# Optimization experiments

Measured on AMD Instinct MI355X. Metric: run time of the kernel, lower is better.

The kernel has to match this reference:

```python
import jax, jax.numpy as jnp
import numpy as np

NEG = jnp.float32(-1e30)  # finite stand-in for -inf (grad-safe)
BLANK = 0


def setup_inputs() -> dict:
    key = jax.random.key(0)
    k1, k2, k3, k4 = jax.random.split(key, 4)
    B, T, V, S = 64, 1024, 128, 256
    logits = jax.random.normal(k1, (B, T, V), dtype=jnp.float32)
    log_probs = jax.nn.log_softmax(logits, axis=-1)  # valid log-probs like a model head
    log_probs_length = jax.random.randint(k2, (B,), 768, T + 1)
    text_encoded = jax.random.randint(k3, (B, S), 1, V)  # labels exclude blank=0
    text_encoded_length = jax.random.randint(k4, (B,), 64, S + 1)
    return {
        "log_probs": log_probs,
        "log_probs_length": log_probs_length,
        "text_encoded": text_encoded,
        "text_encoded_length": text_encoded_length,
    }


def _ctc_loss(log_probs, input_lengths, targets, target_lengths):
    """CTC loss, matching torch.nn.CTCLoss(blank=0, reduction='mean', zero_infinity=True)."""
    B, T, V = log_probs.shape
    S = targets.shape[1]
    L2 = 2 * S + 1  # extended label sequence: blank-interleaved

    # extended labels ext[b, s]: blank at even s, target[(s-1)//2] at odd s
    ext = jnp.full((B, L2), BLANK, dtype=targets.dtype)
    ext = ext.at[:, 1::2].set(targets)

    # gather per-step log-prob of each extended label: [B, T, L2]
    lp_ext = jnp.take_along_axis(
        log_probs, jnp.broadcast_to(ext[:, None, :], (B, T, L2)), axis=2
    )

    pos = jnp.arange(L2)
    valid_s = pos[None, :] < (2 * target_lengths[:, None] + 1)  # [B, L2]
    ext_m2 = jnp.pad(ext, ((0, 0), (2, 0)), constant_values=BLANK)[:, :-2]
    # skip transition s-2 -> s allowed only at non-blank (odd) positions with differing labels
    skip_mask = (pos[None, :] >= 2) & (pos[None, :] % 2 == 1) & (ext != ext_m2)

    alpha0 = jnp.full((B, L2), NEG, dtype=log_probs.dtype)
    alpha0 = alpha0.at[:, 0].set(lp_ext[:, 0, 0])
    alpha0 = alpha0.at[:, 1].set(jnp.where(target_lengths > 0, lp_ext[:, 0, 1], NEG))
    alpha0 = jnp.where(valid_s, alpha0, NEG)

    lp_ext_T = jnp.moveaxis(lp_ext, 1, 0)  # [T, B, L2]

    def step(alpha, x):
        lp_t, t = x
        s1 = jnp.pad(alpha, ((0, 0), (1, 0)), constant_values=NEG)[:, :-1]
        s2 = jnp.pad(alpha, ((0, 0), (2, 0)), constant_values=NEG)[:, :-2]
        a = jnp.logaddexp(alpha, s1)
        a = jnp.where(skip_mask, jnp.logaddexp(a, s2), a)
        new = jnp.where(valid_s, a + lp_t, NEG)
        # freeze alpha for samples whose input sequence has ended
        new = jnp.where((t < input_lengths)[:, None], new, alpha)
        return new, None

    alpha, _ = jax.lax.scan(step, alpha0, (lp_ext_T[1:], jnp.arange(1, T)))

    L = target_lengths
    idx1 = (2 * L)[:, None]
    idx0 = jnp.maximum(2 * L - 1, 0)[:, None]
    a_blank = jnp.take_along_axis(alpha, idx1, axis=1)[:, 0]
    a_label = jnp.take_along_axis(alpha, idx0, axis=1)[:, 0]
    ll = jnp.logaddexp(a_blank, jnp.where(L > 0, a_label, NEG))
    loss_b = -ll
    # zero_infinity: zero out infeasible alignments
    loss_b = jnp.where(loss_b > 1e29, jnp.float32(0.0), loss_b)
    # reduction='mean': divide each loss by its target length, then batch-mean
    return jnp.mean(loss_b / jnp.maximum(L, 1).astype(log_probs.dtype))


def reference(log_probs, log_probs_length, text_encoded, text_encoded_length):
    return _ctc_loss(log_probs, log_probs_length, text_encoded, text_encoded_length)
```

## Files before the change

kernel.cpp:

```cpp
#include <hip/hip_runtime.h>

constexpr int B_ = 64;
constexpr int T_ = 1024;
constexpr int V_ = 128;
constexpr int S_ = 256;
constexpr int GRING = 32;
constexpr int ROWF = 384;
constexpr int NGW = 4;
constexpr float INV_LN2 = 1.4426950408889634f;
constexpr float LN2 = 0.6931471805599453f;
constexpr unsigned MAGIC = 0x5AD0F00Du;

#define WG_SCOPE __HIP_MEMORY_SCOPE_WORKGROUP
#define AG_SCOPE __HIP_MEMORY_SCOPE_AGENT

template<int CTRL>
__device__ __forceinline__ float dppf(float x) {
    return __int_as_float(__builtin_amdgcn_update_dpp(
        0, __float_as_int(x), CTRL, 0xF, 0xF, false));
}
constexpr int DPP_WAVE_SHR1 = 0x138;
constexpr int DPP_WAVE_SHL1 = 0x130;
constexpr int DPP_ROW_SHR1  = 0x111;
constexpr int DPP_ROW_SHR2  = 0x112;
constexpr int DPP_ROW_SHR4  = 0x114;
constexpr int DPP_ROW_SHR8  = 0x118;
constexpr int DPP_BCAST15   = 0x142;
constexpr int DPP_BCAST31   = 0x143;

__device__ __forceinline__ void poll_eq(int* p, int want) {
    while (__hip_atomic_load(p, __ATOMIC_RELAXED, WG_SCOPE) != want)
        __builtin_amdgcn_s_sleep(1);
}
__device__ __forceinline__ void poll_ge(int* p, int want) {
    while (__hip_atomic_load(p, __ATOMIC_RELAXED, WG_SCOPE) < want)
        __builtin_amdgcn_s_sleep(1);
}

__device__ __forceinline__ int wave_rescale(float a[10], int& K) {
    float mx = a[0];
    #pragma unroll
    for (int k = 1; k < 10; ++k) mx = fmaxf(mx, a[k]);
    mx = fmaxf(mx, dppf<DPP_ROW_SHR1>(mx));
    mx = fmaxf(mx, dppf<DPP_ROW_SHR2>(mx));
    mx = fmaxf(mx, dppf<DPP_ROW_SHR4>(mx));
    mx = fmaxf(mx, dppf<DPP_ROW_SHR8>(mx));
    mx = fmaxf(mx, dppf<DPP_BCAST15>(mx));
    mx = fmaxf(mx, dppf<DPP_BCAST31>(mx));
    const unsigned mb = (unsigned)__builtin_amdgcn_readlane(__float_as_uint(mx), 63);
    const int ks = (mb != 0u) ? (250 - (int)(mb >> 23)) : 0;
    #pragma unroll
    for (int k = 0; k < 10; ++k) a[k] = ldexpf(a[k], ks);
    K += ks;
    return ks;
}

__global__ __launch_bounds__(1024) void ctc_fused8(
    const float* __restrict__ lp,
    const int* __restrict__ in_len,
    const int* __restrict__ tgt,
    const int* __restrict__ tgt_len,
    float* __restrict__ wloss,
    int* __restrict__ wflag,
    float* __restrict__ out)
{
    const int b    = blockIdx.x;
    const int tid  = threadIdx.x;
    const int wid  = tid >> 6;
    const int lane = tid & 63;

    __shared__ float ringF[GRING * ROWF];
    __shared__ float ringB[GRING * ROWF];
    __shared__ float dumpB[640];
    __shared__ int   tagF[8], tagB[8];
    __shared__ int   consF, consB;
    __shared__ int   KBsh;

    const int L  = tgt_len[b];
    const int Tb = in_len[b];
    const float* lpb = lp + (size_t)b * T_ * V_;
    const int* tg = tgt + b * S_;

    const int tm = (Tb - 2) >> 1;
    const int Uf = tm;
    const int Ub = Tb - 2 - tm;

    if (tid == 0) { consF = 0; consB = 0; }
    if (tid < 8) tagF[tid] = -1;
    else if (tid < 16) tagB[tid - 8] = -1;
    __syncthreads();

    if (wid == 4 || wid == 5 || wid == 8 || wid == 9 || wid == 12 || wid == 13)
        return;

    if (wid >= 2) {
        const int gi  = (wid >> 2) * 2 + (wid & 1);
        const int dir = (gi >= 4) ? 1 : 0;
        const int q   = dir ? (gi - 4) : gi;
        const int U   = dir ? Ub : Uf;
        float* ring   = dir ? ringB : ringF;
        int*   tags   = dir ? tagB  : tagF;
        int*   consp  = dir ? &consB : &consF;

        int   labE[5];
        float vmask[5];
        #pragma unroll
        for (int c = 0; c < 5; ++c) {
            const int j = 5 * lane + c;
            if (j < L) { labE[c] = tg[j]; vmask[c] = 1.0f; }
            else       { labE[c] = 0;     vmask[c] = 0.0f; }
        }

        float vA[4][6], vB[4][6];
        auto issueLoads = [&](float (&v)[4][6], int m) {
            const int n = min(4, U - 4 * m);
            #pragma unroll
            for (int r = 0; r < 4; ++r) {
                if (r < n) {
                    const int u = 4 * m + 1 + r;
                    const int t = dir ? (Tb - 1 - u) : u;
                    const float* row = lpb + (size_t)t * V_;
                    v[r][0] = row[0];
                    #pragma unroll
                    for (int c = 0; c < 5; ++c) v[r][c + 1] = row[labE[c]];
                }
            }
        };
        auto processBlock = [&](float (&v)[4][6], int m) {
            const int n = min(4, U - 4 * m);
            while (__hip_atomic_load(consp, __ATOMIC_RELAXED, WG_SCOPE) < 4 * m - 28)
                __builtin_amdgcn_s_sleep(1);
            #pragma unroll
            for (int r = 0; r < 4; ++r) {
                if (r < n) {
                    const int u = 4 * m + 1 + r;
                    float e[6];
                    e[0] = __builtin_exp2f(v[r][0] * INV_LN2);
                    #pragma unroll
                    for (int c = 0; c < 5; ++c)
                        e[c + 1] = vmask[c] * __builtin_exp2f(v[r][c + 1] * INV_LN2);
                    float* rb = ring + ((u - 1) & (GRING - 1)) * ROWF;
                    ((float2*)rb)[lane]         = make_float2(e[0], e[1]);
                    ((float2*)(rb + 128))[lane] = make_float2(e[2], e[3]);
                    ((float2*)(rb + 256))[lane] = make_float2(e[4], e[5]);
                }
            }
            if (lane == 0)
                __hip_atomic_store(&tags[m & 7], m, __ATOMIC_RELEASE, WG_SCOPE);
        };

        int mA = q;
        bool haveA = (4 * mA + 1 <= U);
        if (haveA) issueLoads(vA, mA);
        while (haveA) {
            const int mB = mA + NGW;
            const bool haveB = (4 * mB + 1 <= U);
            if (haveB) issueLoads(vB, mB);
            processBlock(vA, mA);
            const int mA2 = mB + NGW;
            const bool haveA2 = (4 * mA2 + 1 <= U);
            if (haveA2) issueLoads(vA, mA2);
            if (haveB) processBlock(vB, mB);
            mA = mA2; haveA = haveA2;
        }
        return;
    }

    if (wid == 1) {
        float sB[5];
        #pragma unroll
        for (int c = 0; c < 5; ++c) {
            const int j = 5 * lane + c + 1;
            sB[c] = (j < L && tg[j] != tg[j - 1]) ? 1.0f : 0.0f;
        }
        float g[10];
        #pragma unroll
        for (int k = 0; k < 10; ++k) g[k] = 0.0f;
        {
            const float pb = __builtin_exp2f(lpb[(size_t)(Tb - 1) * V_] * INV_LN2);
            const float pl = __builtin_exp2f(lpb[(size_t)(Tb - 1) * V_ + tg[L - 1]] * INV_LN2);
            #pragma unroll
            for (int k = 0; k < 10; ++k) {
                const int s = 10 * lane + k;
                if (s == 2 * L)     g[k] = pb;
                if (s == 2 * L - 1) g[k] = pl;
            }
        }
        float d0n = dppf<DPP_WAVE_SHL1>(g[0]);
        float d1n = dppf<DPP_WAVE_SHL1>(g[1]);
        int K = 0;

        float2 S0[12], S1[12];
        auto readBlock = [&](float2 (&S)[12], int m) {
            const int base = ((4 * m) & (GRING - 1)) * ROWF + 2 * lane;
            #pragma unroll
            for (int r = 0; r < 4; ++r)
                #pragma unroll
                for (int pl = 0; pl < 3; ++pl)
                    S[r * 3 + pl] = *(const float2*)&ringB[base + r * ROWF + pl * 128];
        };
        auto rowCore = [&](float2 c0, float2 c1, float2 c2) {
            const float d0 = d0n, d1 = d1n;
            const float p0 = c0.x;
            g[0] = (g[0] + g[1]) * p0;
            g[1] = (g[1] + g[2] + sB[0] * g[3]) * c0.y;
            d0n = dppf<DPP_WAVE_SHL1>(g[0]);
            d1n = dppf<DPP_WAVE_SHL1>(g[1]);
            g[2] = (g[2] + g[3]) * p0;
            g[3] = (g[3] + g[4] + sB[1] * g[5]) * c1.x;
            g[4] = (g[4] + g[5]) * p0;
            g[5] = (g[5] + g[6] + sB[2] * g[7]) * c1.y;
            g[6] = (g[6] + g[7]) * p0;
            g[7] = (g[7] + g[8] + sB[3] * g[9]) * c2.x;
            g[8] = (g[8] + g[9]) * p0;
            g[9] = (g[9] + d0 + sB[4] * d1) * c2.y;
        };
        auto row4 = [&](float2 (&S)[12]) {
            #pragma unroll
            for (int r = 0; r < 4; ++r) rowCore(S[r * 3], S[r * 3 + 1], S[r * 3 + 2]);
        };

        const int FB = Ub >> 2;
        poll_eq(&tagB[0], 0); readBlock(S0, 0);
        int mb = 0;
        for (; mb + 2 <= FB; mb += 2) {
            if (mb + 1 < FB) { poll_eq(&tagB[(mb + 1) & 7], mb + 1); readBlock(S1, mb + 1); }
            row4(S0);
            if (lane == 0) __hip_atomic_store(&consB, 4 * mb + 4, __ATOMIC_RELAXED, WG_SCOPE);
            if (mb + 2 < FB) { poll_eq(&tagB[(mb + 2) & 7], mb + 2); readBlock(S0, mb + 2); }
            row4(S1);
            if (lane == 0) __hip_atomic_store(&consB, 4 * mb + 8, __ATOMIC_RELAXED, WG_SCOPE);
            { const int ks = wave_rescale(g, K);
              d0n = ldexpf(d0n, ks); d1n = ldexpf(d1n, ks); }
        }
        if (mb < FB) {
            row4(S0);
            if (lane == 0) __hip_atomic_store(&consB, 4 * mb + 4, __ATOMIC_RELAXED, WG_SCOPE);
            { const int ks = wave_rescale(g, K);
              d0n = ldexpf(d0n, ks); d1n = ldexpf(d1n, ks); }
        }
        for (int u = 4 * FB + 1; u <= Ub; ++u) {
            poll_eq(&tagB[FB & 7], FB);
            const int base = ((u - 1) & (GRING - 1)) * ROWF + 2 * lane;
            rowCore(*(const float2*)&ringB[base],
                    *(const float2*)&ringB[base + 128],
                    *(const float2*)&ringB[base + 256]);
        }

        {
            const float d0 = d0n, d1 = d1n;
            g[0] = g[0] + g[1];
            g[1] = g[1] + g[2] + sB[0] * g[3];
            g[2] = g[2] + g[3];
            g[3] = g[3] + g[4] + sB[1] * g[5];
            g[4] = g[4] + g[5];
            g[5] = g[5] + g[6] + sB[2] * g[7];
            g[6] = g[6] + g[7];
            g[7] = g[7] + g[8] + sB[3] * g[9];
            g[8] = g[8] + g[9];
            g[9] = g[9] + d0 + sB[4] * d1;
        }
        #pragma unroll
        for (int k = 0; k < 10; ++k) dumpB[10 * lane + k] = g[k];
        if (lane == 0) {
            KBsh = K;
            __hip_atomic_store(&consB, Ub + 64, __ATOMIC_RELAXED, WG_SCOPE);
        }
        return;
    }

    float skipf[5];
    #pragma unroll
    for (int c = 0; c < 5; ++c) {
        const int j = 5 * lane + c;
        skipf[c] = (j >= 1 && j < L && tg[j] != tg[j - 1]) ? 1.0f : 0.0f;
    }
    float a[10];
    #pragma unroll
    for (int k = 0; k < 10; ++k) a[k] = 0.0f;
    {
        const float p00 = __builtin_exp2f(lpb[0] * INV_LN2);
        const float p01 = __builtin_exp2f(lpb[tg[0]] * INV_LN2);
        if (lane == 0) { a[0] = p00; a[1] = p01; }
    }
    float u9n = 0.0f;
    int K = 0;

    float2 S0[12], S1[12];
    auto readBlock = [&](float2 (&S)[12], int m) {
        const int base = ((4 * m) & (GRING - 1)) * ROWF + 2 * lane;
        #pragma unroll
        for (int r = 0; r < 4; ++r)
            #pragma unroll
            for (int pl = 0; pl < 3; ++pl)
                S[r * 3 + pl] = *(const float2*)&ringF[base + r * ROWF + pl * 128];
    };
    auto rowCore = [&](float2 c0, float2 c1, float2 c2) {
        const float u9 = u9n;
        const float p0 = c0.x;
        a[9] = (a[9] + a[8] + skipf[4] * a[7]) * c2.y;
        u9n = dppf<DPP_WAVE_SHR1>(a[9]);
        a[8] = (a[8] + a[7]) * p0;
        a[7] = (a[7] + a[6] + skipf[3] * a[5]) * c2.x;
        a[6] = (a[6] + a[5]) * p0;
        a[5] = (a[5] + a[4] + skipf[2] * a[3]) * c1.y;
        a[4] = (a[4] + a[3]) * p0;
        a[3] = (a[3] + a[2] + skipf[1] * a[1]) * c1.x;
        a[2] = (a[2] + a[1]) * p0;
        a[1] = (a[1] + a[0] + skipf[0] * u9) * c0.y;
        a[0] = (a[0] + u9) * p0;
    };
    auto row4 = [&](float2 (&S)[12]) {
        #pragma unroll
        for (int r = 0; r < 4; ++r) rowCore(S[r * 3], S[r * 3 + 1], S[r * 3 + 2]);
    };

    const int FB = Uf >> 2;
    poll_eq(&tagF[0], 0); readBlock(S0, 0);
    int mb = 0;
    for (; mb + 2 <= FB; mb += 2) {
        if (mb + 1 < FB) { poll_eq(&tagF[(mb + 1) & 7], mb + 1); readBlock(S1, mb + 1); }
        row4(S0);
        if (lane == 0) __hip_atomic_store(&consF, 4 * mb + 4, __ATOMIC_RELAXED, WG_SCOPE);
        if (mb + 2 < FB) { poll_eq(&tagF[(mb + 2) & 7], mb + 2); readBlock(S0, mb + 2); }
        row4(S1);
        if (lane == 0) __hip_atomic_store(&consF, 4 * mb + 8, __ATOMIC_RELAXED, WG_SCOPE);
        { const int ks = wave_rescale(a, K); u9n = ldexpf(u9n, ks); }
    }
    if (mb < FB) {
        row4(S0);
        if (lane == 0) __hip_atomic_store(&consF, 4 * mb + 4, __ATOMIC_RELAXED, WG_SCOPE);
        { const int ks = wave_rescale(a, K); u9n = ldexpf(u9n, ks); }
    }
    for (int u = 4 * FB + 1; u <= Uf; ++u) {
        poll_eq(&tagF[FB & 7], FB);
        const int base = ((u - 1) & (GRING - 1)) * ROWF + 2 * lane;
        rowCore(*(const float2*)&ringF[base],
                *(const float2*)&ringF[base + 128],
                *(const float2*)&ringF[base + 256]);
    }
    if (lane == 0) __hip_atomic_store(&consF, Uf + 64, __ATOMIC_RELAXED, WG_SCOPE);

    poll_ge(&consB, Ub + 64);
    double sum = 0.0;
    #pragma unroll
    for (int k = 0; k < 10; ++k)
        sum += (double)a[k] * (double)dumpB[10 * lane + k];
    #pragma unroll
    for (int d = 1; d < 64; d <<= 1) sum += __shfl_xor(sum, d, 64);

    if (lane == 0) {
        float loss = 0.0f;
        if (sum > 0.0) {
            const long long ub2 = __double_as_longlong(sum);
            const int ex = (int)((ub2 >> 52) & 2047) - 1023;
            const double f = __longlong_as_double(
                (ub2 & 0x000FFFFFFFFFFFFFLL) | 0x3FF0000000000000LL);
            const float ll2 = __builtin_log2f((float)f) + (float)(ex - K - KBsh);
            loss = -(ll2 * LN2);
            if (!(loss <= 1e29f)) loss = 0.0f;
        }
        wloss[b] = loss / (float)L;
        __hip_atomic_store(&wflag[b], (int)MAGIC, __ATOMIC_RELEASE, AG_SCOPE);
    }

    if (b == 0) {
        while ((unsigned)__hip_atomic_load(&wflag[lane], __ATOMIC_ACQUIRE, AG_SCOPE) != MAGIC)
            __builtin_amdgcn_s_sleep(1);
        float v = wloss[lane];
        #pragma unroll
        for (int o = 1; o < 64; o <<= 1) v += __shfl_xor(v, o, 64);
        if (lane == 0) out[0] = v / (float)B_;
    }
}

extern "C" void kernel_launch(void* const* d_in, const int* in_sizes, int n_in,
                              void* d_out, int out_size, void* d_ws, size_t ws_size,
                              hipStream_t stream) {
    const float* lp      = (const float*)d_in[0];
    const int*   in_len  = (const int*)d_in[1];
    const int*   tgt     = (const int*)d_in[2];
    const int*   tgt_len = (const int*)d_in[3];
    float* wloss = (float*)d_ws;
    int*   wflag = (int*)((char*)d_ws + 256);
    float* out   = (float*)d_out;

    ctc_fused8<<<B_, 1024, 0, stream>>>(lp, in_len, tgt, tgt_len, wloss, wflag, out);
}
```

Measured before the change: 142.9 us.

## Load full log-prob rows coalesced, gather labels via bpermute, and speculate ring tag polls

Producer waves now load each time step's 128-wide log-prob row as one coalesced float2 per lane. The per-label values are gathered in-register with ds_bpermute instead of six scattered global loads per lane. Consumer waves read the ring tag for the next block before computing the current one and skip the blocking poll when the tag is already set, so the synchronisation latency sits off the critical recurrence. The trade is extra bpermute and select work in the producer in return for fewer uncoalesced loads and less polling stall in the serial alpha and beta loops.

Measured after the change: 142.4 us. About the same (-0.4%).

```diff
diff --git a/kernel.cpp b/kernel.cpp
--- a/kernel.cpp
+++ b/kernel.cpp
@@ -28,6 +28,10 @@
 constexpr int DPP_BCAST15   = 0x142;
 constexpr int DPP_BCAST31   = 0x143;
 
+__device__ __forceinline__ float bperm(int byte_idx, float v) {
+    return __int_as_float(__builtin_amdgcn_ds_bpermute(byte_idx, __float_as_int(v)));
+}
+
 __device__ __forceinline__ void poll_eq(int* p, int want) {
     while (__hip_atomic_load(p, __ATOMIC_RELAXED, WG_SCOPE) != want)
         __builtin_amdgcn_s_sleep(1);
@@ -55,7 +59,7 @@
     return ks;
 }
 
-__global__ __launch_bounds__(1024) void ctc_fused8(
+__global__ __launch_bounds__(1024) void ctc_fused9(
     const float* __restrict__ lp,
     const int* __restrict__ in_len,
     const int* __restrict__ tgt,
@@ -102,31 +106,31 @@
         int*   tags   = dir ? tagB  : tagF;
         int*   consp  = dir ? &consB : &consF;
 
-        int   labE[5];
+        int   bidx[5];
+        float oddc[5];
         float vmask[5];
         #pragma unroll
         for (int c = 0; c < 5; ++c) {
             const int j = 5 * lane + c;
-            if (j < L) { labE[c] = tg[j]; vmask[c] = 1.0f; }
-            else       { labE[c] = 0;     vmask[c] = 0.0f; }
-        }
-
-        float vA[4][6], vB[4][6];
-        auto issueLoads = [&](float (&v)[4][6], int m) {
+            const int lab = (j < L) ? tg[j] : 0;
+            bidx[c]  = (lab >> 1) << 2;
+            oddc[c]  = (lab & 1) ? 1.0f : 0.0f;
+            vmask[c] = (j < L) ? 1.0f : 0.0f;
+        }
+
+        float2 vA[4], vB[4];
+        auto issueLoads = [&](float2 (&v)[4], int m) {
             const int n = min(4, U - 4 * m);
             #pragma unroll
             for (int r = 0; r < 4; ++r) {
                 if (r < n) {
                     const int u = 4 * m + 1 + r;
                     const int t = dir ? (Tb - 1 - u) : u;
-                    const float* row = lpb + (size_t)t * V_;
-                    v[r][0] = row[0];
-                    #pragma unroll
-                    for (int c = 0; c < 5; ++c) v[r][c + 1] = row[labE[c]];
+                    v[r] = ((const float2*)(lpb + (size_t)t * V_))[lane];
                 }
             }
         };
-        auto processBlock = [&](float (&v)[4][6], int m) {
+        auto processBlock = [&](float2 (&v)[4], int m) {
             const int n = min(4, U - 4 * m);
             while (__hip_atomic_load(consp, __ATOMIC_RELAXED, WG_SCOPE) < 4 * m - 28)
                 __builtin_amdgcn_s_sleep(1);
@@ -135,10 +139,14 @@
                 if (r < n) {
                     const int u = 4 * m + 1 + r;
                     float e[6];
-                    e[0] = __builtin_exp2f(v[r][0] * INV_LN2);
+                    e[0] = __builtin_exp2f(bperm(0, v[r].x) * INV_LN2);
                     #pragma unroll
-                    for (int c = 0; c < 5; ++c)
-                        e[c + 1] = vmask[c] * __builtin_exp2f(v[r][c + 1] * INV_LN2);
+                    for (int c = 0; c < 5; ++c) {
+                        const float va = bperm(bidx[c], v[r].x);
+                        const float vb = bperm(bidx[c], v[r].y);
+                        const float val = va + oddc[c] * (vb - va);
+                        e[c + 1] = vmask[c] * __builtin_exp2f(val * INV_LN2);
+                    }
                     float* rb = ring + ((u - 1) & (GRING - 1)) * ROWF;
                     ((float2*)rb)[lane]         = make_float2(e[0], e[1]);
                     ((float2*)(rb + 128))[lane] = make_float2(e[2], e[3]);
@@ -224,14 +232,24 @@
         poll_eq(&tagB[0], 0); readBlock(S0, 0);
         int mb = 0;
         for (; mb + 2 <= FB; mb += 2) {
-            if (mb + 1 < FB) { poll_eq(&tagB[(mb + 1) & 7], mb + 1); readBlock(S1, mb + 1); }
+            if (mb + 1 < FB) readBlock(S1, mb + 1);
+            int spA = (mb + 2 < FB)
+                ? __hip_atomic_load(&tagB[(mb + 2) & 7], __ATOMIC_RELAXED, WG_SCOPE) : 0;
+            __builtin_amdgcn_sched_barrier(0);
             row4(S0);
             if (lane == 0) __hip_atomic_store(&consB, 4 * mb + 4, __ATOMIC_RELAXED, WG_SCOPE);
-            if (mb + 2 < FB) { poll_eq(&tagB[(mb + 2) & 7], mb + 2); readBlock(S0, mb + 2); }
+            if (mb + 2 < FB) {
+                if (spA != mb + 2) poll_eq(&tagB[(mb + 2) & 7], mb + 2);
+                readBlock(S0, mb + 2);
+            }
+            int spB = (mb + 3 < FB)
+                ? __hip_atomic_load(&tagB[(mb + 3) & 7], __ATOMIC_RELAXED, WG_SCOPE) : 0;
+            __builtin_amdgcn_sched_barrier(0);
             row4(S1);
             if (lane == 0) __hip_atomic_store(&consB, 4 * mb + 8, __ATOMIC_RELAXED, WG_SCOPE);
             { const int ks = wave_rescale(g, K);
               d0n = ldexpf(d0n, ks); d1n = ldexpf(d1n, ks); }
+            if (mb + 3 < FB && spB != mb + 3) poll_eq(&tagB[(mb + 3) & 7], mb + 3);
         }
         if (mb < FB) {
             row4(S0);
@@ -319,13 +337,23 @@
     poll_eq(&tagF[0], 0); readBlock(S0, 0);
     int mb = 0;
     for (; mb + 2 <= FB; mb += 2) {
-        if (mb + 1 < FB) { poll_eq(&tagF[(mb + 1) & 7], mb + 1); readBlock(S1, mb + 1); }
+        if (mb + 1 < FB) readBlock(S1, mb + 1);
+        int spA = (mb + 2 < FB)
+            ? __hip_atomic_load(&tagF[(mb + 2) & 7], __ATOMIC_RELAXED, WG_SCOPE) : 0;
+        __builtin_amdgcn_sched_barrier(0);
         row4(S0);
         if (lane == 0) __hip_atomic_store(&consF, 4 * mb + 4, __ATOMIC_RELAXED, WG_SCOPE);
-        if (mb + 2 < FB) { poll_eq(&tagF[(mb + 2) & 7], mb + 2); readBlock(S0, mb + 2); }
+        if (mb + 2 < FB) {
+            if (spA != mb + 2) poll_eq(&tagF[(mb + 2) & 7], mb + 2);
+            readBlock(S0, mb + 2);
+        }
+        int spB = (mb + 3 < FB)
+            ? __hip_atomic_load(&tagF[(mb + 3) & 7], __ATOMIC_RELAXED, WG_SCOPE) : 0;
+        __builtin_amdgcn_sched_barrier(0);
         row4(S1);
         if (lane == 0) __hip_atomic_store(&consF, 4 * mb + 8, __ATOMIC_RELAXED, WG_SCOPE);
         { const int ks = wave_rescale(a, K); u9n = ldexpf(u9n, ks); }
+        if (mb + 3 < FB && spB != mb + 3) poll_eq(&tagF[(mb + 3) & 7], mb + 3);
     }
     if (mb < FB) {
         row4(S0);
@@ -385,5 +413,5 @@
     int*   wflag = (int*)((char*)d_ws + 256);
     float* out   = (float*)d_out;
 
-    ctc_fused8<<<B_, 1024, 0, stream>>>(lp, in_len, tgt, tgt_len, wloss, wflag, out);
-}
+    ctc_fused9<<<B_, 1024, 0, stream>>>(lp, in_len, tgt, tgt_len, wloss, wflag, out);
+}
```

## Drop producer waves and shared ring; recurrence waves load log-probs directly

Applied to the files above, without the earlier changes.

Removes the eight producer waves that gathered log-probs, exponentiated them and pushed them through shared-memory rings with tag/consumer polling. The forward and backward recurrence waves now gather their own rows from global memory, software-prefetched two 4-row blocks ahead, and compute exp inline. The block shrinks from 1024 to 128 threads and most shared memory is freed. The goal is to eliminate the polling and LDS handoff latency. The risk is that global-load latency and exp work now sit on the serial critical path of each recurrence wave.

New measurement: 186.1 us. +30.2%, slower.

```diff
diff --git a/kernel.cpp b/kernel.cpp
--- a/kernel.cpp
+++ b/kernel.cpp
@@ -4,9 +4,6 @@
 constexpr int T_ = 1024;
 constexpr int V_ = 128;
 constexpr int S_ = 256;
-constexpr int GRING = 32;
-constexpr int ROWF = 384;
-constexpr int NGW = 4;
 constexpr float INV_LN2 = 1.4426950408889634f;
 constexpr float LN2 = 0.6931471805599453f;
 constexpr unsigned MAGIC = 0x5AD0F00Du;
@@ -28,15 +25,6 @@
 constexpr int DPP_BCAST15   = 0x142;
 constexpr int DPP_BCAST31   = 0x143;
 
-__device__ __forceinline__ void poll_eq(int* p, int want) {
-    while (__hip_atomic_load(p, __ATOMIC_RELAXED, WG_SCOPE) != want)
-        __builtin_amdgcn_s_sleep(1);
-}
-__device__ __forceinline__ void poll_ge(int* p, int want) {
-    while (__hip_atomic_load(p, __ATOMIC_RELAXED, WG_SCOPE) < want)
-        __builtin_amdgcn_s_sleep(1);
-}
-
 __device__ __forceinline__ int wave_rescale(float a[10], int& K) {
     float mx = a[0];
     #pragma unroll
@@ -55,7 +43,7 @@
     return ks;
 }
 
-__global__ __launch_bounds__(1024) void ctc_fused8(
+__global__ __launch_bounds__(128) void ctc_direct(
     const float* __restrict__ lp,
     const int* __restrict__ in_len,
     const int* __restrict__ tgt,
@@ -69,11 +57,8 @@
     const int wid  = tid >> 6;
     const int lane = tid & 63;
 
-    __shared__ float ringF[GRING * ROWF];
-    __shared__ float ringB[GRING * ROWF];
     __shared__ float dumpB[640];
-    __shared__ int   tagF[8], tagB[8];
-    __shared__ int   consF, consB;
+    __shared__ int   consB;
     __shared__ int   KBsh;
 
     const int L  = tgt_len[b];
@@ -85,93 +70,21 @@
     const int Uf = tm;
     const int Ub = Tb - 2 - tm;
 
-    if (tid == 0) { consF = 0; consB = 0; }
-    if (tid < 8) tagF[tid] = -1;
-    else if (tid < 16) tagB[tid - 8] = -1;
+    if (tid == 0) consB = 0;
     __syncthreads();
 
-    if (wid == 4 || wid == 5 || wid == 8 || wid == 9 || wid == 12 || wid == 13)
-        return;
-
-    if (wid >= 2) {
-        const int gi  = (wid >> 2) * 2 + (wid & 1);
-        const int dir = (gi >= 4) ? 1 : 0;
-        const int q   = dir ? (gi - 4) : gi;
-        const int U   = dir ? Ub : Uf;
-        float* ring   = dir ? ringB : ringF;
-        int*   tags   = dir ? tagB  : tagF;
-        int*   consp  = dir ? &consB : &consF;
-
+    if (wid == 1) {
+        const int U = Ub;
         int   labE[5];
         float vmask[5];
+        float sB[5];
         #pragma unroll
         for (int c = 0; c < 5; ++c) {
             const int j = 5 * lane + c;
-            if (j < L) { labE[c] = tg[j]; vmask[c] = 1.0f; }
-            else       { labE[c] = 0;     vmask[c] = 0.0f; }
-        }
-
-        float vA[4][6], vB[4][6];
-        auto issueLoads = [&](float (&v)[4][6], int m) {
-            const int n = min(4, U - 4 * m);
-            #pragma unroll
-            for (int r = 0; r < 4; ++r) {
-                if (r < n) {
-                    const int u = 4 * m + 1 + r;
-                    const int t = dir ? (Tb - 1 - u) : u;
-                    const float* row = lpb + (size_t)t * V_;
-                    v[r][0] = row[0];
-                    #pragma unroll
-                    for (int c = 0; c < 5; ++c) v[r][c + 1] = row[labE[c]];
-                }
-            }
-        };
-        auto processBlock = [&](float (&v)[4][6], int m) {
-            const int n = min(4, U - 4 * m);
-            while (__hip_atomic_load(consp, __ATOMIC_RELAXED, WG_SCOPE) < 4 * m - 28)
-                __builtin_amdgcn_s_sleep(1);
-            #pragma unroll
-            for (int r = 0; r < 4; ++r) {
-                if (r < n) {
-                    const int u = 4 * m + 1 + r;
-                    float e[6];
-                    e[0] = __builtin_exp2f(v[r][0] * INV_LN2);
-                    #pragma unroll
-                    for (int c = 0; c < 5; ++c)
-                        e[c + 1] = vmask[c] * __builtin_exp2f(v[r][c + 1] * INV_LN2);
-                    float* rb = ring + ((u - 1) & (GRING - 1)) * ROWF;
-                    ((float2*)rb)[lane]         = make_float2(e[0], e[1]);
-                    ((float2*)(rb + 128))[lane] = make_float2(e[2], e[3]);
-                    ((float2*)(rb + 256))[lane] = make_float2(e[4], e[5]);
-                }
-            }
-            if (lane == 0)
-                __hip_atomic_store(&tags[m & 7], m, __ATOMIC_RELEASE, WG_SCOPE);
-        };
-
-        int mA = q;
-        bool haveA = (4 * mA + 1 <= U);
-        if (haveA) issueLoads(vA, mA);
-        while (haveA) {
-            const int mB = mA + NGW;
-            const bool haveB = (4 * mB + 1 <= U);
-            if (haveB) issueLoads(vB, mB);
-            processBlock(vA, mA);
-            const int mA2 = mB + NGW;
-            const bool haveA2 = (4 * mA2 + 1 <= U);
-            if (haveA2) issueLoads(vA, mA2);
-            if (haveB) processBlock(vB, mB);
-            mA = mA2; haveA = haveA2;
-        }
-        return;
-    }
-
-    if (wid == 1) {
-        float sB[5];
-        #pragma unroll
-        for (int c = 0; c < 5; ++c) {
-            const int j = 5 * lane + c + 1;
-            sB[c] = (j < L && tg[j] != tg[j - 1]) ? 1.0f : 0.0f;
+            labE[c]  = (j < L) ? tg[j] : 0;
+            vmask[c] = (j < L) ? 1.0f : 0.0f;
+            const int j2 = j + 1;
+            sB[c] = (j2 < L && tg[j2] != tg[j2 - 1]) ? 1.0f : 0.0f;
         }
         float g[10];
         #pragma unroll
@@ -190,61 +103,66 @@
         float d1n = dppf<DPP_WAVE_SHL1>(g[1]);
         int K = 0;
 
-        float2 S0[12], S1[12];
-        auto readBlock = [&](float2 (&S)[12], int m) {
-            const int base = ((4 * m) & (GRING - 1)) * ROWF + 2 * lane;
-            #pragma unroll
-            for (int r = 0; r < 4; ++r)
+        float G0[24], G1[24];
+        auto issue = [&](float (&G)[24], int m) {
+            #pragma unroll
+            for (int r = 0; r < 4; ++r) {
+                int u = 4 * m + 1 + r; u = (u <= U) ? u : U;
+                const float* row = lpb + (size_t)(Tb - 1 - u) * V_;
+                G[6 * r] = row[0];
                 #pragma unroll
-                for (int pl = 0; pl < 3; ++pl)
-                    S[r * 3 + pl] = *(const float2*)&ringB[base + r * ROWF + pl * 128];
+                for (int c = 0; c < 5; ++c) G[6 * r + 1 + c] = row[labE[c]];
+            }
         };
-        auto rowCore = [&](float2 c0, float2 c1, float2 c2) {
+        auto rowCore = [&](float p0, float q1, float q3, float q5, float q7, float q9) {
             const float d0 = d0n, d1 = d1n;
-            const float p0 = c0.x;
             g[0] = (g[0] + g[1]) * p0;
-            g[1] = (g[1] + g[2] + sB[0] * g[3]) * c0.y;
+            g[1] = (g[1] + g[2] + sB[0] * g[3]) * q1;
             d0n = dppf<DPP_WAVE_SHL1>(g[0]);
             d1n = dppf<DPP_WAVE_SHL1>(g[1]);
             g[2] = (g[2] + g[3]) * p0;
-            g[3] = (g[3] + g[4] + sB[1] * g[5]) * c1.x;
+            g[3] = (g[3] + g[4] + sB[1] * g[5]) * q3;
             g[4] = (g[4] + g[5]) * p0;
-            g[5] = (g[5] + g[6] + sB[2] * g[7]) * c1.y;
+            g[5] = (g[5] + g[6] + sB[2] * g[7]) * q5;
             g[6] = (g[6] + g[7]) * p0;
-            g[7] = (g[7] + g[8] + sB[3] * g[9]) * c2.x;
+            g[7] = (g[7] + g[8] + sB[3] * g[9]) * q7;
             g[8] = (g[8] + g[9]) * p0;
-            g[9] = (g[9] + d0 + sB[4] * d1) * c2.y;
+            g[9] = (g[9] + d0 + sB[4] * d1) * q9;
         };
-        auto row4 = [&](float2 (&S)[12]) {
-            #pragma unroll
-            for (int r = 0; r < 4; ++r) rowCore(S[r * 3], S[r * 3 + 1], S[r * 3 + 2]);
+        auto proc4 = [&](const float (&G)[24]) {
+            #pragma unroll
+            for (int r = 0; r < 4; ++r) {
+                float e[6];
+                e[0] = __builtin_exp2f(G[6 * r] * INV_LN2);
+                #pragma unroll
+                for (int c = 0; c < 5; ++c)
+                    e[c + 1] = vmask[c] * __builtin_exp2f(G[6 * r + 1 + c] * INV_LN2);
+                rowCore(e[0], e[1], e[2], e[3], e[4], e[5]);
+            }
         };
 
-        const int FB = Ub >> 2;
-        poll_eq(&tagB[0], 0); readBlock(S0, 0);
+        const int FB = U >> 2;
+        issue(G0, 0); issue(G1, 1);
         int mb = 0;
         for (; mb + 2 <= FB; mb += 2) {
-            if (mb + 1 < FB) { poll_eq(&tagB[(mb + 1) & 7], mb + 1); readBlock(S1, mb + 1); }
-            row4(S0);
-            if (lane == 0) __hip_atomic_store(&consB, 4 * mb + 4, __ATOMIC_RELAXED, WG_SCOPE);
-            if (mb + 2 < FB) { poll_eq(&tagB[(mb + 2) & 7], mb + 2); readBlock(S0, mb + 2); }
-            row4(S1);
-            if (lane == 0) __hip_atomic_store(&consB, 4 * mb + 8, __ATOMIC_RELAXED, WG_SCOPE);
+            proc4(G0); issue(G0, mb + 2);
+            proc4(G1); issue(G1, mb + 3);
             { const int ks = wave_rescale(g, K);
               d0n = ldexpf(d0n, ks); d1n = ldexpf(d1n, ks); }
         }
         if (mb < FB) {
-            row4(S0);
-            if (lane == 0) __hip_atomic_store(&consB, 4 * mb + 4, __ATOMIC_RELAXED, WG_SCOPE);
+            proc4(G0);
             { const int ks = wave_rescale(g, K);
               d0n = ldexpf(d0n, ks); d1n = ldexpf(d1n, ks); }
         }
-        for (int u = 4 * FB + 1; u <= Ub; ++u) {
-            poll_eq(&tagB[FB & 7], FB);
-            const int base = ((u - 1) & (GRING - 1)) * ROWF + 2 * lane;
-            rowCore(*(const float2*)&ringB[base],
-                    *(const float2*)&ringB[base + 128],
-                    *(const float2*)&ringB[base + 256]);
+        for (int u = 4 * FB + 1; u <= U; ++u) {
+            const float* row = lpb + (size_t)(Tb - 1 - u) * V_;
+            float e[6];
+            e[0] = __builtin_exp2f(row[0] * INV_LN2);
+            #pragma unroll
+            for (int c = 0; c < 5; ++c)
+                e[c + 1] = vmask[c] * __builtin_exp2f(row[labE[c]] * INV_LN2);
+            rowCore(e[0], e[1], e[2], e[3], e[4], e[5]);
         }
 
         {
@@ -264,15 +182,20 @@
         for (int k = 0; k < 10; ++k) dumpB[10 * lane + k] = g[k];
         if (lane == 0) {
             KBsh = K;
-            __hip_atomic_store(&consB, Ub + 64, __ATOMIC_RELAXED, WG_SCOPE);
+            __hip_atomic_store(&consB, 1, __ATOMIC_RELAXED, WG_SCOPE);
         }
         return;
     }
 
+    const int U = Uf;
+    int   labE[5];
+    float vmask[5];
     float skipf[5];
     #pragma unroll
     for (int c = 0; c < 5; ++c) {
         const int j = 5 * lane + c;
+        labE[c]  = (j < L) ? tg[j] : 0;
+        vmask[c] = (j < L) ? 1.0f : 0.0f;
         skipf[c] = (j >= 1 && j < L && tg[j] != tg[j - 1]) ? 1.0f : 0.0f;
     }
     float a[10];
@@ -286,62 +209,67 @@
     float u9n = 0.0f;
     int K = 0;
 
-    float2 S0[12], S1[12];
-    auto readBlock = [&](float2 (&S)[12], int m) {
-        const int base = ((4 * m) & (GRING - 1)) * ROWF + 2 * lane;
-        #pragma unroll
-        for (int r = 0; r < 4; ++r)
-            #pragma unroll
-            for (int pl = 0; pl < 3; ++pl)
-                S[r * 3 + pl] = *(const float2*)&ringF[base + r * ROWF + pl * 128];
+    float G0[24], G1[24];
+    auto issue = [&](float (&G)[24], int m) {
+        #pragma unroll
+        for (int r = 0; r < 4; ++r) {
+            int u = 4 * m + 1 + r; u = (u <= U) ? u : U;
+            const float* row = lpb + (size_t)u * V_;
+            G[6 * r] = row[0];
+            #pragma unroll
+            for (int c = 0; c < 5; ++c) G[6 * r + 1 + c] = row[labE[c]];
+        }
     };
-    auto rowCore = [&](float2 c0, float2 c1, float2 c2) {
+    auto rowCore = [&](float p0, float q1, float q3, float q5, float q7, float q9) {
         const float u9 = u9n;
-        const float p0 = c0.x;
-        a[9] = (a[9] + a[8] + skipf[4] * a[7]) * c2.y;
+        a[9] = (a[9] + a[8] + skipf[4] * a[7]) * q9;
         u9n = dppf<DPP_WAVE_SHR1>(a[9]);
         a[8] = (a[8] + a[7]) * p0;
-        a[7] = (a[7] + a[6] + skipf[3] * a[5]) * c2.x;
+        a[7] = (a[7] + a[6] + skipf[3] * a[5]) * q7;
         a[6] = (a[6] + a[5]) * p0;
-        a[5] = (a[5] + a[4] + skipf[2] * a[3]) * c1.y;
+        a[5] = (a[5] + a[4] + skipf[2] * a[3]) * q5;
         a[4] = (a[4] + a[3]) * p0;
-        a[3] = (a[3] + a[2] + skipf[1] * a[1]) * c1.x;
+        a[3] = (a[3] + a[2] + skipf[1] * a[1]) * q3;
         a[2] = (a[2] + a[1]) * p0;
-        a[1] = (a[1] + a[0] + skipf[0] * u9) * c0.y;
+        a[1] = (a[1] + a[0] + skipf[0] * u9) * q1;
         a[0] = (a[0] + u9) * p0;
     };
-    auto row4 = [&](float2 (&S)[12]) {
-        #pragma unroll
-        for (int r = 0; r < 4; ++r) rowCore(S[r * 3], S[r * 3 + 1], S[r * 3 + 2]);
+    auto proc4 = [&](const float (&G)[24]) {
+        #pragma unroll
+        for (int r = 0; r < 4; ++r) {
+            float e[6];
+            e[0] = __builtin_exp2f(G[6 * r] * INV_LN2);
+            #pragma unroll
+            for (int c = 0; c < 5; ++c)
+                e[c + 1] = vmask[c] * __builtin_exp2f(G[6 * r + 1 + c] * INV_LN2);
+            rowCore(e[0], e[1], e[2], e[3], e[4], e[5]);
+        }
     };
 
-    const int FB = Uf >> 2;
-    poll_eq(&tagF[0], 0); readBlock(S0, 0);
+    const int FB = U >> 2;
+    issue(G0, 0); issue(G1, 1);
     int mb = 0;
     for (; mb + 2 <= FB; mb += 2) {
-        if (mb + 1 < FB) { poll_eq(&tagF[(mb + 1) & 7], mb + 1); readBlock(S1, mb + 1); }
-        row4(S0);
-        if (lane == 0) __hip_atomic_store(&consF, 4 * mb + 4, __ATOMIC_RELAXED, WG_SCOPE);
-        if (mb + 2 < FB) { poll_eq(&tagF[(mb + 2) & 7], mb + 2); readBlock(S0, mb + 2); }
-        row4(S1);
-        if (lane == 0) __hip_atomic_store(&consF, 4 * mb + 8, __ATOMIC_RELAXED, WG_SCOPE);
+        proc4(G0); issue(G0, mb + 2);
+        proc4(G1); issue(G1, mb + 3);
         { const int ks = wave_rescale(a, K); u9n = ldexpf(u9n, ks); }
     }
     if (mb < FB) {
-        row4(S0);
-        if (lane == 0) __hip_atomic_store(&consF, 4 * mb + 4, __ATOMIC_RELAXED, WG_SCOPE);
+        proc4(G0);
         { const int ks = wave_rescale(a, K); u9n = ldexpf(u9n, ks); }
     }
-    for (int u = 4 * FB + 1; u <= Uf; ++u) {
-        poll_eq(&tagF[FB & 7], FB);
-        const int base = ((u - 1) & (GRING - 1)) * ROWF + 2 * lane;
-        rowCore(*(const float2*)&ringF[base],
-                *(const float2*)&ringF[base + 128],
-                *(const float2*)&ringF[base + 256]);
-    }
-    if (lane == 0) __hip_atomic_store(&consF, Uf + 64, __ATOMIC_RELAXED, WG_SCOPE);
-
-    poll_ge(&consB, Ub + 64);
+    for (int u = 4 * FB + 1; u <= U; ++u) {
+        const float* row = lpb + (size_t)u * V_;
+        float e[6];
+        e[0] = __builtin_exp2f(row[0] * INV_LN2);
+        #pragma unroll
+        for (int c = 0; c < 5; ++c)
+            e[c + 1] = vmask[c] * __builtin_exp2f(row[labE[c]] * INV_LN2);
+        rowCore(e[0], e[1], e[2], e[3], e[4], e[5]);
+    }
+
+    while (__hip_atomic_load(&consB, __ATOMIC_RELAXED, WG_SCOPE) != 1)
+        __builtin_amdgcn_s_sleep(1);
     double sum = 0.0;
     #pragma unroll
     for (int k = 0; k < 10; ++k)
@@ -385,5 +313,5 @@
     int*   wflag = (int*)((char*)d_ws + 256);
     float* out   = (float*)d_out;
 
-    ctc_fused8<<<B_, 1024, 0, stream>>>(lp, in_len, tgt, tgt_len, wloss, wflag, out);
+    ctc_direct<<<B_, 128, 0, stream>>>(lp, in_len, tgt, tgt_len, wloss, wflag, out);
 }
```
